# Kernel tuning notes

Measured on AMD Instinct MI355X. Metric: run time of the kernel, lower is better.

Reference implementation:

```python
import jax, jax.numpy as jnp
import numpy as np

N_NODES = 50000
N_EDGES = 600000
N_GRAPHS = 64


def _linear_init(key, fan_in, fan_out):
    # torch nn.Linear default: U(-1/sqrt(fan_in), 1/sqrt(fan_in))
    s = 1.0 / np.sqrt(fan_in)
    kw, kb = jax.random.split(key)
    W = jax.random.uniform(kw, (fan_in, fan_out), jnp.float32, -s, s)
    b = jax.random.uniform(kb, (fan_out,), jnp.float32, -s, s)
    return W, b


def setup_inputs() -> dict:
    key = jax.random.key(0)
    ks = jax.random.split(key, 7)
    x = jax.random.normal(ks[0], (N_NODES, 128), jnp.float32)
    edge_index = jax.random.randint(ks[1], (2, N_EDGES), 0, N_NODES, dtype=jnp.int32).astype(jnp.int64)
    batch = jnp.sort(jax.random.randint(ks[2], (N_NODES,), 0, N_GRAPHS, dtype=jnp.int32)).astype(jnp.int64)
    W1, b1 = _linear_init(ks[3], 128, 256)
    W2, b2 = _linear_init(ks[4], 256, 256)
    W3, b3 = _linear_init(ks[5], 256, 128)
    W4, b4 = _linear_init(ks[6], 128, 10)
    return dict(x=x, edge_index=edge_index, batch=batch,
                W1=W1, b1=b1, W2=W2, b2=b2, W3=W3, b3=b3, W4=W4, b4=b4)


def _gcn_conv(h, src, dst, W, b, n_nodes):
    # PyG GCNConv: add self-loops (src/dst already include them),
    # symmetric normalization D^{-1/2} (A+I) D^{-1/2} h W + b.
    h = h @ W                                      # [N, Cout]
    deg = jax.ops.segment_sum(jnp.ones(src.shape[0], h.dtype), dst, num_segments=n_nodes)
    dinv = jnp.where(deg > 0, jax.lax.rsqrt(deg), 0.0)
    norm = dinv[src] * dinv[dst]                   # [E+N]
    msg = h[src] * norm[:, None]                   # gather + scale per edge
    agg = jax.ops.segment_sum(msg, dst, num_segments=n_nodes)  # scatter-add
    return agg + b


def reference(x, edge_index, batch, W1, b1, W2, b2, W3, b3, W4, b4):
    n = x.shape[0]
    loops = jnp.arange(n, dtype=edge_index.dtype)
    src = jnp.concatenate([edge_index[0], loops])
    dst = jnp.concatenate([edge_index[1], loops])
    # GCNBlock (activate_last=True since dense layers follow)
    h = jax.nn.relu(_gcn_conv(x, src, dst, W1, b1, n))
    h = jax.nn.relu(_gcn_conv(h, src, dst, W2, b2, n))
    # global_mean_pool over batch segments
    sums = jax.ops.segment_sum(h, batch, num_segments=N_GRAPHS)          # [G, 256]
    counts = jax.ops.segment_sum(jnp.ones((n,), h.dtype), batch, num_segments=N_GRAPHS)
    g = sums / jnp.maximum(counts, 1.0)[:, None]
    # DenseBlock [256 -> 128 -> 10], activate_last=False
    g = jax.nn.relu(g @ W3 + b3)
    return g @ W4 + b4
```

## Files before the change

### kernel.cpp

```cpp
#include <hip/hip_runtime.h>

typedef unsigned short u16;
typedef unsigned int u32;
typedef __attribute__((ext_vector_type(8))) short s16x8;
typedef __attribute__((ext_vector_type(4))) float f32x4;

#define NN 50000
#define NE 600000
#define NG 64

__device__ __forceinline__ u16 f2bf(float f) {
    u32 u = __float_as_uint(f);
    u32 r = (u + 0x7fffu + ((u >> 16) & 1u)) >> 16;
    return (u16)r;
}
__device__ __forceinline__ float bf2f(u16 h) {
    return __uint_as_float(((u32)h) << 16);
}
__device__ __forceinline__ void gll16(const void* g, void* l) {
    __builtin_amdgcn_global_load_lds((const __attribute__((address_space(1))) u32*)g,
                                     (__attribute__((address_space(3))) u32*)l, 16, 0, 0);
}

__global__ void k_hist(const int* __restrict__ dst, int* __restrict__ cnt, int ne) {
    int e = blockIdx.x * blockDim.x + threadIdx.x;
    if (e < ne) atomicAdd(&cnt[dst[e]], 1);
}

__global__ __launch_bounds__(256)
void k_scan1(const int* __restrict__ cnt, int* __restrict__ bsum, int n) {
    int i = blockIdx.x * 256 + threadIdx.x;
    int v = (i < n) ? cnt[i] : 0;
#pragma unroll
    for (int off = 32; off > 0; off >>= 1) v += __shfl_down(v, off, 64);
    __shared__ int ws[4];
    int lane = threadIdx.x & 63, w = threadIdx.x >> 6;
    if (lane == 0) ws[w] = v;
    __syncthreads();
    if (threadIdx.x == 0) bsum[blockIdx.x] = ws[0] + ws[1] + ws[2] + ws[3];
}

__global__ __launch_bounds__(256)
void k_scan2(int* __restrict__ bsum, int nb) {
    int t = threadIdx.x;
    int v = (t < nb) ? bsum[t] : 0;
    int lane = t & 63, w = t >> 6;
    int inc = v;
#pragma unroll
    for (int off = 1; off < 64; off <<= 1) {
        int x = __shfl_up(inc, off, 64);
        if (lane >= off) inc += x;
    }
    __shared__ int wtot[4];
    if (lane == 63) wtot[w] = inc;
    __syncthreads();
    int wo = 0;
    for (int j = 0; j < w; ++j) wo += wtot[j];
    if (t < nb) bsum[t] = wo + inc - v;
}

__global__ __launch_bounds__(256)
void k_scan3(const int* __restrict__ cnt, const int* __restrict__ boff,
             int* __restrict__ rowptr, int* __restrict__ cursor,
             float* __restrict__ dinv, int n) {
    int i = blockIdx.x * 256 + threadIdx.x;
    int v = (i < n) ? cnt[i] : 0;
    int lane = threadIdx.x & 63, w = threadIdx.x >> 6;
    int inc = v;
#pragma unroll
    for (int off = 1; off < 64; off <<= 1) {
        int x = __shfl_up(inc, off, 64);
        if (lane >= off) inc += x;
    }
    __shared__ int wtot[4];
    if (lane == 63) wtot[w] = inc;
    __syncthreads();
    int wo = boff[blockIdx.x];
    for (int j = 0; j < w; ++j) wo += wtot[j];
    if (i < n) {
        int excl = wo + inc - v;
        rowptr[i] = excl;
        cursor[i] = excl;
        dinv[i] = rsqrtf(1.0f + (float)v);
        if (i == n - 1) rowptr[n] = excl + v;
    }
}

__global__ void k_fill(const int* __restrict__ src, const int* __restrict__ dst,
                       const float* __restrict__ dinv,
                       int* __restrict__ cursor, uint2* __restrict__ csr2, int ne) {
    int e = blockIdx.x * blockDim.x + threadIdx.x;
    if (e < ne) {
        int pos = atomicAdd(&cursor[dst[e]], 1);
        int s = src[e];
        csr2[pos] = make_uint2((u32)s, __float_as_uint(dinv[s]));
    }
}

__device__ __forceinline__ void wsplit_tiled(const float* __restrict__ W,
                                             u16* __restrict__ hi, int gid) {
    int n = gid & 255, kgrp = gid >> 8;
    int kbase = kgrp * 8;
#pragma unroll
    for (int j = 0; j < 8; ++j) {
        float w = W[(size_t)(kbase + j) * 256 + n];
        hi[(size_t)gid * 8 + j] = f2bf(w);
    }
}

__global__ __launch_bounds__(256)
void k_preamble(const float* __restrict__ x, u16* __restrict__ xbf,
                const float* __restrict__ W1, u16* __restrict__ w1hi,
                const float* __restrict__ W2, u16* __restrict__ w2hi,
                float* __restrict__ sums, int* __restrict__ cnt,
                const int* __restrict__ batch, float* __restrict__ counts) {
    const int XB = (NN * 32 + 255) / 256;
    const int CB = (NN + 255) / 256;
    int b = blockIdx.x, t = threadIdx.x;
    if (b < XB) {
        int i = b * 256 + t;
        if (i < NN * 32) {
            float4 v = ((const float4*)x)[i];
            ushort4 o;
            o.x = f2bf(v.x); o.y = f2bf(v.y); o.z = f2bf(v.z); o.w = f2bf(v.w);
            ((ushort4*)xbf)[i] = o;
        }
        return;
    }
    b -= XB;
    if (b < 16) { wsplit_tiled(W1, w1hi, b * 256 + t); return; }
    b -= 16;
    if (b < 32) { wsplit_tiled(W2, w2hi, b * 256 + t); return; }
    b -= 32;
    if (b < 64) { sums[b * 256 + t] = 0.f; return; }
    b -= 64;
    if (b < CB) {
        int i = b * 256 + t;
        if (i < NN) cnt[i] = 0;
        return;
    }
    b -= CB;
    if (b == 0) {
        __shared__ int lb[65];
        if (t <= 64) {
            int lo = 0, hi = NN;
            while (lo < hi) {
                int mid = (lo + hi) >> 1;
                if (batch[mid] < t) lo = mid + 1; else hi = mid;
            }
            lb[t] = lo;
        }
        __syncthreads();
        if (t < 64) counts[t] = (float)(lb[t + 1] - lb[t]);
    }
}

__device__ __forceinline__ void fma8(float* a, const uint4& v, float w) {
    a[0] += bf2f((u16)v.x) * w; a[1] += bf2f((u16)(v.x >> 16)) * w;
    a[2] += bf2f((u16)v.y) * w; a[3] += bf2f((u16)(v.y >> 16)) * w;
    a[4] += bf2f((u16)v.z) * w; a[5] += bf2f((u16)(v.z >> 16)) * w;
    a[6] += bf2f((u16)v.w) * w; a[7] += bf2f((u16)(v.w >> 16)) * w;
}
__device__ __forceinline__ void fma4(float* a, const uint2& v, float w) {
    a[0] += bf2f((u16)v.x) * w; a[1] += bf2f((u16)(v.x >> 16)) * w;
    a[2] += bf2f((u16)v.y) * w; a[3] += bf2f((u16)(v.y >> 16)) * w;
}

template<int C>
__global__ __launch_bounds__(256)
void k_agg_gather(const int* __restrict__ rowptr, const uint2* __restrict__ csr2,
                  const float* __restrict__ dinv, const u16* __restrict__ hb,
                  u16* __restrict__ out, int n) {
    constexpr int VL = C / 32;
    int tid = threadIdx.x;
    int node = (blockIdx.x * 256 + tid) >> 5;
    if (node >= n) return;
    int sl = tid & 31;
    int beg = rowptr[node];
    int m = rowptr[node + 1] - beg;
    float di = dinv[node];
    float a0[VL], a1[VL];
    if constexpr (VL == 8) {
        uint4 v = ((const uint4*)hb)[(size_t)node * 32 + sl];
#pragma unroll
        for (int i = 0; i < 8; ++i) a1[i] = 0.f;
        a0[0] = bf2f((u16)v.x) * di; a0[1] = bf2f((u16)(v.x >> 16)) * di;
        a0[2] = bf2f((u16)v.y) * di; a0[3] = bf2f((u16)(v.y >> 16)) * di;
        a0[4] = bf2f((u16)v.z) * di; a0[5] = bf2f((u16)(v.z >> 16)) * di;
        a0[6] = bf2f((u16)v.w) * di; a0[7] = bf2f((u16)(v.w >> 16)) * di;
    } else {
        uint2 v = ((const uint2*)hb)[(size_t)node * 32 + sl];
#pragma unroll
        for (int i = 0; i < 4; ++i) a1[i] = 0.f;
        a0[0] = bf2f((u16)v.x) * di; a0[1] = bf2f((u16)(v.x >> 16)) * di;
        a0[2] = bf2f((u16)v.y) * di; a0[3] = bf2f((u16)(v.y >> 16)) * di;
    }
    const uint2* ep = csr2 + beg;
    int e = 0;
    for (; e + 4 <= m; e += 4) {
        uint2 e0 = ep[e], e1 = ep[e + 1], e2 = ep[e + 2], e3 = ep[e + 3];
        float w0 = __uint_as_float(e0.y), w1 = __uint_as_float(e1.y);
        float w2 = __uint_as_float(e2.y), w3 = __uint_as_float(e3.y);
        if constexpr (VL == 8) {
            uint4 r0 = ((const uint4*)hb)[(size_t)e0.x * 32 + sl];
            uint4 r1 = ((const uint4*)hb)[(size_t)e1.x * 32 + sl];
            uint4 r2 = ((const uint4*)hb)[(size_t)e2.x * 32 + sl];
            uint4 r3 = ((const uint4*)hb)[(size_t)e3.x * 32 + sl];
            fma8(a0, r0, w0); fma8(a1, r1, w1); fma8(a0, r2, w2); fma8(a1, r3, w3);
        } else {
            uint2 r0 = ((const uint2*)hb)[(size_t)e0.x * 32 + sl];
            uint2 r1 = ((const uint2*)hb)[(size_t)e1.x * 32 + sl];
            uint2 r2 = ((const uint2*)hb)[(size_t)e2.x * 32 + sl];
            uint2 r3 = ((const uint2*)hb)[(size_t)e3.x * 32 + sl];
            fma4(a0, r0, w0); fma4(a1, r1, w1); fma4(a0, r2, w2); fma4(a1, r3, w3);
        }
    }
    for (; e < m; ++e) {
        uint2 e0 = ep[e];
        float w0 = __uint_as_float(e0.y);
        if constexpr (VL == 8) {
            uint4 r0 = ((const uint4*)hb)[(size_t)e0.x * 32 + sl];
            fma8(a0, r0, w0);
        } else {
            uint2 r0 = ((const uint2*)hb)[(size_t)e0.x * 32 + sl];
            fma4(a0, r0, w0);
        }
    }
    if constexpr (VL == 8) {
        uint4 o;
        o.x = (u32)f2bf((a0[0] + a1[0]) * di) | ((u32)f2bf((a0[1] + a1[1]) * di) << 16);
        o.y = (u32)f2bf((a0[2] + a1[2]) * di) | ((u32)f2bf((a0[3] + a1[3]) * di) << 16);
        o.z = (u32)f2bf((a0[4] + a1[4]) * di) | ((u32)f2bf((a0[5] + a1[5]) * di) << 16);
        o.w = (u32)f2bf((a0[6] + a1[6]) * di) | ((u32)f2bf((a0[7] + a1[7]) * di) << 16);
        ((uint4*)out)[(size_t)node * 32 + sl] = o;
    } else {
        uint2 o;
        o.x = (u32)f2bf((a0[0] + a1[0]) * di) | ((u32)f2bf((a0[1] + a1[1]) * di) << 16);
        o.y = (u32)f2bf((a0[2] + a1[2]) * di) | ((u32)f2bf((a0[3] + a1[3]) * di) << 16);
        ((uint2*)out)[(size_t)node * 32 + sl] = o;
    }
}

template<bool POOL>
__global__ __launch_bounds__(512, 4)
void k_gemm_mfma(const u16* __restrict__ A, const u16* __restrict__ Bh,
                 const float* __restrict__ bias, u16* __restrict__ out_bf,
                 const int* __restrict__ batch, float* __restrict__ pool,
                 int M, int K) {
    __shared__ u16 ldsA[2][4096];
    const int tid = threadIdx.x, lane = tid & 63, wid = tid >> 6;
    const int bm = blockIdx.x * 128;
    const int wr = (wid >> 2) * 64, wc = (wid & 3) * 64;
    const int lr = lane & 15, kg = lane >> 4;

    const int srow = wid * 16 + (lane >> 2);
    const int sslot = lane & 3;
    const int ssw = (srow ^ (srow >> 2)) & 3;
    int srg = bm + srow; if (srg >= M) srg = M - 1;
    const u16* sbase = A + (size_t)srg * K + ((sslot ^ ssw) << 3);

    const u16* bh_p = Bh + (u32)kg * 2048 + (u32)(wc + lr) * 8;

    f32x4 acc[4][4];
#pragma unroll
    for (int i = 0; i < 4; ++i)
#pragma unroll
        for (int j = 0; j < 4; ++j) acc[i][j] = (f32x4){0.f, 0.f, 0.f, 0.f};

    const int nt = K >> 5;
    gll16(sbase, &ldsA[0][wid * 512]);
    __syncthreads();

    for (int t = 0; t < nt; ++t) {
        int cur = t & 1;
        if (t + 1 < nt)
            gll16(sbase + ((t + 1) << 5), &ldsA[cur ^ 1][wid * 512]);

        s16x8 bh[4];
#pragma unroll
        for (int fn = 0; fn < 4; ++fn)
            bh[fn] = *(const s16x8*)&bh_p[(u32)t * 8192 + (u32)fn * 128];
        const u16* lb = ldsA[cur];
        s16x8 a[4];
#pragma unroll
        for (int fm = 0; fm < 4; ++fm) {
            int r = wr + fm * 16 + lr;
            a[fm] = *(const s16x8*)&lb[r * 32 + ((kg ^ ((r ^ (r >> 2)) & 3)) << 3)];
        }
#pragma unroll
        for (int fn = 0; fn < 4; ++fn)
#pragma unroll
            for (int fm = 0; fm < 4; ++fm)
                acc[fm][fn] = __builtin_amdgcn_mfma_f32_16x16x32_bf16(a[fm], bh[fn], acc[fm][fn], 0, 0, 0);
        __syncthreads();
    }

#pragma unroll
    for (int fn = 0; fn < 4; ++fn) {
        int col = wc + fn * 16 + lr;
        float bv = bias[col];
        if (!POOL) {
#pragma unroll
            for (int fm = 0; fm < 4; ++fm) {
                int rbase = bm + wr + fm * 16 + kg * 4;
#pragma unroll
                for (int r = 0; r < 4; ++r) {
                    int row = rbase + r;
                    if (row < M)
                        out_bf[(size_t)row * 256 + col] = f2bf(fmaxf(acc[fm][fn][r] + bv, 0.f));
                }
            }
        } else {
            int gcur = -1;
            float run = 0.f;
#pragma unroll
            for (int fm = 0; fm < 4; ++fm) {
                int rbase = bm + wr + fm * 16 + kg * 4;
#pragma unroll
                for (int r = 0; r < 4; ++r) {
                    int row = rbase + r;
                    if (row < M) {
                        int g = batch[row];
                        float v = fmaxf(acc[fm][fn][r] + bv, 0.f);
                        if (g != gcur) {
                            if (gcur >= 0) atomicAdd(&pool[gcur * 256 + col], run);
                            gcur = g;
                            run = 0.f;
                        }
                        run += v;
                    }
                }
            }
            if (gcur >= 0) atomicAdd(&pool[gcur * 256 + col], run);
        }
    }
}

__global__ __launch_bounds__(128)
void k_dense(const float* __restrict__ sums, const float* __restrict__ counts,
             const float* __restrict__ W3, const float* __restrict__ b3,
             const float* __restrict__ W4, const float* __restrict__ b4,
             float* __restrict__ out) {
    __shared__ float g[256];
    __shared__ float hid[128];
    int gi = blockIdx.x;
    int t = threadIdx.x;
    float inv = 1.0f / fmaxf(counts[gi], 1.0f);
    for (int c = t; c < 256; c += 128) g[c] = sums[gi * 256 + c] * inv;
    __syncthreads();
    float acc = b3[t];
    for (int k = 0; k < 256; ++k) acc += g[k] * W3[k * 128 + t];
    hid[t] = fmaxf(acc, 0.0f);
    __syncthreads();
    if (t < 10) {
        float o = b4[t];
        for (int k = 0; k < 128; ++k) o += hid[k] * W4[k * 10 + t];
        out[gi * 10 + t] = o;
    }
}

extern "C" void kernel_launch(void* const* d_in, const int* in_sizes, int n_in,
                              void* d_out, int out_size, void* d_ws, size_t ws_size,
                              hipStream_t stream) {
    const float* x   = (const float*)d_in[0];
    const int*  eidx = (const int*)d_in[1];
    const int*  batch= (const int*)d_in[2];
    const float* W1 = (const float*)d_in[3];
    const float* b1 = (const float*)d_in[4];
    const float* W2 = (const float*)d_in[5];
    const float* b2 = (const float*)d_in[6];
    const float* W3 = (const float*)d_in[7];
    const float* b3 = (const float*)d_in[8];
    const float* W4 = (const float*)d_in[9];
    const float* b4 = (const float*)d_in[10];
    float* out = (float*)d_out;

    const int N = NN, E = NE, G = NG;
    const int* src = eidx;
    const int* dst = eidx + E;
    const int NB = (N + 255) / 256;

    char* p = (char*)d_ws;
    auto alloc = [&](size_t bytes) { char* r = p; p += (bytes + 255) & ~(size_t)255; return r; };
    u16*   h1bf   = (u16*)alloc((size_t)N * 256 * 2);
    u16*   xbf    = (u16*)alloc((size_t)N * 128 * 2);
    float* dinv   = (float*)alloc((size_t)N * 4);
    float* sums   = (float*)alloc((size_t)G * 256 * 4);
    float* counts = (float*)alloc((size_t)G * 4);
    int*   cnt    = (int*)alloc((size_t)N * 4);
    int*   rowptr = (int*)alloc((size_t)(N + 1) * 4);
    int*   bsum   = (int*)alloc((size_t)NB * 4);
    uint2* csr2   = (uint2*)alloc((size_t)E * 8);
    u16*   agg1   = (u16*)alloc((size_t)N * 128 * 2);
    u16*   agg2   = (u16*)alloc((size_t)N * 256 * 2);
    u16*   w1hi   = (u16*)alloc((size_t)256 * 128 * 2);
    u16*   w2hi   = (u16*)alloc((size_t)256 * 256 * 2);
    int*   cursor = cnt;

    const int XB = (NN * 32 + 255) / 256;
    const int CB = (NN + 255) / 256;
    int pre_blocks = XB + 16 + 32 + 64 + CB + 1;
    k_preamble<<<pre_blocks, 256, 0, stream>>>(x, xbf, W1, w1hi, W2, w2hi,
                                               sums, cnt, batch, counts);

    k_hist<<<(E + 255) / 256, 256, 0, stream>>>(dst, cnt, E);
    k_scan1<<<NB, 256, 0, stream>>>(cnt, bsum, N);
    k_scan2<<<1, 256, 0, stream>>>(bsum, NB);
    k_scan3<<<NB, 256, 0, stream>>>(cnt, bsum, rowptr, cursor, dinv, N);
    k_fill<<<(E + 255) / 256, 256, 0, stream>>>(src, dst, dinv, cursor, csr2, E);

    k_agg_gather<128><<<(N + 7) / 8, 256, 0, stream>>>(rowptr, csr2, dinv, xbf, agg1, N);
    int gblocks = (N + 127) / 128;
    k_gemm_mfma<false><<<gblocks, 512, 0, stream>>>(agg1, w1hi, b1, h1bf,
                                                    nullptr, nullptr, N, 128);

    k_agg_gather<256><<<(N + 7) / 8, 256, 0, stream>>>(rowptr, csr2, dinv, h1bf, agg2, N);
    k_gemm_mfma<true><<<gblocks, 512, 0, stream>>>(agg2, w2hi, b2, nullptr,
                                                   batch, sums, N, 256);

    k_dense<<<G, 128, 0, stream>>>(sums, counts, W3, b3, W4, b4, out);
}
```

Measured before the change: 215.3 us.

## Fuse neighbor aggregation into MFMA GEMM via LDS-resident aggregated tile

Merges the sparse gather-aggregate kernel with the following MFMA GEMM: each 512-thread block aggregates its 128 nodes directly into a swizzled LDS tile holding the full K width, then runs the GEMM from LDS without double-buffered global loads. This removes the write and re-read of the intermediate aggregated feature buffers and two kernel launches. In exchange, LDS use grows to 64 KB for K=256, which may cut occupancy, and the irregular gather phase no longer overlaps with MFMA work inside a block.

New measurement: 220.5 us. 1.02x slower.

```diff
diff --git a/kernel.cpp b/kernel.cpp
--- a/kernel.cpp
+++ b/kernel.cpp
@@ -16,10 +16,6 @@
 }
 __device__ __forceinline__ float bf2f(u16 h) {
     return __uint_as_float(((u32)h) << 16);
-}
-__device__ __forceinline__ void gll16(const void* g, void* l) {
-    __builtin_amdgcn_global_load_lds((const __attribute__((address_space(1))) u32*)g,
-                                     (__attribute__((address_space(3))) u32*)l, 16, 0, 0);
 }
 
 __global__ void k_hist(const int* __restrict__ dst, int* __restrict__ cnt, int ne) {
@@ -166,99 +162,95 @@
     a[2] += bf2f((u16)v.y) * w; a[3] += bf2f((u16)(v.y >> 16)) * w;
 }
 
-template<int C>
-__global__ __launch_bounds__(256)
-void k_agg_gather(const int* __restrict__ rowptr, const uint2* __restrict__ csr2,
-                  const float* __restrict__ dinv, const u16* __restrict__ hb,
-                  u16* __restrict__ out, int n) {
-    constexpr int VL = C / 32;
-    int tid = threadIdx.x;
-    int node = (blockIdx.x * 256 + tid) >> 5;
-    if (node >= n) return;
-    int sl = tid & 31;
-    int beg = rowptr[node];
-    int m = rowptr[node + 1] - beg;
-    float di = dinv[node];
-    float a0[VL], a1[VL];
-    if constexpr (VL == 8) {
-        uint4 v = ((const uint4*)hb)[(size_t)node * 32 + sl];
-#pragma unroll
-        for (int i = 0; i < 8; ++i) a1[i] = 0.f;
-        a0[0] = bf2f((u16)v.x) * di; a0[1] = bf2f((u16)(v.x >> 16)) * di;
-        a0[2] = bf2f((u16)v.y) * di; a0[3] = bf2f((u16)(v.y >> 16)) * di;
-        a0[4] = bf2f((u16)v.z) * di; a0[5] = bf2f((u16)(v.z >> 16)) * di;
-        a0[6] = bf2f((u16)v.w) * di; a0[7] = bf2f((u16)(v.w >> 16)) * di;
-    } else {
-        uint2 v = ((const uint2*)hb)[(size_t)node * 32 + sl];
-#pragma unroll
-        for (int i = 0; i < 4; ++i) a1[i] = 0.f;
-        a0[0] = bf2f((u16)v.x) * di; a0[1] = bf2f((u16)(v.x >> 16)) * di;
-        a0[2] = bf2f((u16)v.y) * di; a0[3] = bf2f((u16)(v.y >> 16)) * di;
-    }
-    const uint2* ep = csr2 + beg;
-    int e = 0;
-    for (; e + 4 <= m; e += 4) {
-        uint2 e0 = ep[e], e1 = ep[e + 1], e2 = ep[e + 2], e3 = ep[e + 3];
-        float w0 = __uint_as_float(e0.y), w1 = __uint_as_float(e1.y);
-        float w2 = __uint_as_float(e2.y), w3 = __uint_as_float(e3.y);
-        if constexpr (VL == 8) {
-            uint4 r0 = ((const uint4*)hb)[(size_t)e0.x * 32 + sl];
-            uint4 r1 = ((const uint4*)hb)[(size_t)e1.x * 32 + sl];
-            uint4 r2 = ((const uint4*)hb)[(size_t)e2.x * 32 + sl];
-            uint4 r3 = ((const uint4*)hb)[(size_t)e3.x * 32 + sl];
-            fma8(a0, r0, w0); fma8(a1, r1, w1); fma8(a0, r2, w2); fma8(a1, r3, w3);
-        } else {
-            uint2 r0 = ((const uint2*)hb)[(size_t)e0.x * 32 + sl];
-            uint2 r1 = ((const uint2*)hb)[(size_t)e1.x * 32 + sl];
-            uint2 r2 = ((const uint2*)hb)[(size_t)e2.x * 32 + sl];
-            uint2 r3 = ((const uint2*)hb)[(size_t)e3.x * 32 + sl];
-            fma4(a0, r0, w0); fma4(a1, r1, w1); fma4(a0, r2, w2); fma4(a1, r3, w3);
-        }
-    }
-    for (; e < m; ++e) {
-        uint2 e0 = ep[e];
-        float w0 = __uint_as_float(e0.y);
-        if constexpr (VL == 8) {
-            uint4 r0 = ((const uint4*)hb)[(size_t)e0.x * 32 + sl];
-            fma8(a0, r0, w0);
-        } else {
-            uint2 r0 = ((const uint2*)hb)[(size_t)e0.x * 32 + sl];
-            fma4(a0, r0, w0);
-        }
-    }
-    if constexpr (VL == 8) {
-        uint4 o;
-        o.x = (u32)f2bf((a0[0] + a1[0]) * di) | ((u32)f2bf((a0[1] + a1[1]) * di) << 16);
-        o.y = (u32)f2bf((a0[2] + a1[2]) * di) | ((u32)f2bf((a0[3] + a1[3]) * di) << 16);
-        o.z = (u32)f2bf((a0[4] + a1[4]) * di) | ((u32)f2bf((a0[5] + a1[5]) * di) << 16);
-        o.w = (u32)f2bf((a0[6] + a1[6]) * di) | ((u32)f2bf((a0[7] + a1[7]) * di) << 16);
-        ((uint4*)out)[(size_t)node * 32 + sl] = o;
-    } else {
-        uint2 o;
-        o.x = (u32)f2bf((a0[0] + a1[0]) * di) | ((u32)f2bf((a0[1] + a1[1]) * di) << 16);
-        o.y = (u32)f2bf((a0[2] + a1[2]) * di) | ((u32)f2bf((a0[3] + a1[3]) * di) << 16);
-        ((uint2*)out)[(size_t)node * 32 + sl] = o;
-    }
-}
-
-template<bool POOL>
+template<bool POOL, int K>
 __global__ __launch_bounds__(512, 4)
-void k_gemm_mfma(const u16* __restrict__ A, const u16* __restrict__ Bh,
-                 const float* __restrict__ bias, u16* __restrict__ out_bf,
-                 const int* __restrict__ batch, float* __restrict__ pool,
-                 int M, int K) {
-    __shared__ u16 ldsA[2][4096];
+void k_fused(const int* __restrict__ rowptr, const uint2* __restrict__ csr2,
+             const float* __restrict__ dinv, const u16* __restrict__ hb,
+             const u16* __restrict__ Bh, const float* __restrict__ bias,
+             u16* __restrict__ out_bf, const int* __restrict__ batch,
+             float* __restrict__ pool, int M) {
+    __shared__ u16 ldsA[128 * K];
     const int tid = threadIdx.x, lane = tid & 63, wid = tid >> 6;
     const int bm = blockIdx.x * 128;
+    constexpr int VL = K / 32;
+
+    {
+        int sl = lane & 31;
+        int half = lane >> 5;
+        for (int it = 0; it < 8; ++it) {
+            int row = wid * 16 + it * 2 + half;
+            int node = bm + row; if (node >= M) node = M - 1;
+            int beg = rowptr[node];
+            int m = rowptr[node + 1] - beg;
+            float di = dinv[node];
+            float a0[VL], a1[VL];
+            if constexpr (VL == 8) {
+                uint4 v = ((const uint4*)hb)[(size_t)node * 32 + sl];
+#pragma unroll
+                for (int i = 0; i < 8; ++i) a1[i] = 0.f;
+                a0[0] = bf2f((u16)v.x) * di; a0[1] = bf2f((u16)(v.x >> 16)) * di;
+                a0[2] = bf2f((u16)v.y) * di; a0[3] = bf2f((u16)(v.y >> 16)) * di;
+                a0[4] = bf2f((u16)v.z) * di; a0[5] = bf2f((u16)(v.z >> 16)) * di;
+                a0[6] = bf2f((u16)v.w) * di; a0[7] = bf2f((u16)(v.w >> 16)) * di;
+            } else {
+                uint2 v = ((const uint2*)hb)[(size_t)node * 32 + sl];
+#pragma unroll
+                for (int i = 0; i < 4; ++i) a1[i] = 0.f;
+                a0[0] = bf2f((u16)v.x) * di; a0[1] = bf2f((u16)(v.x >> 16)) * di;
+                a0[2] = bf2f((u16)v.y) * di; a0[3] = bf2f((u16)(v.y >> 16)) * di;
+            }
+            const uint2* ep = csr2 + beg;
+            int e = 0;
+            for (; e + 4 <= m; e += 4) {
+                uint2 e0 = ep[e], e1 = ep[e + 1], e2 = ep[e + 2], e3 = ep[e + 3];
+                float w0 = __uint_as_float(e0.y), w1 = __uint_as_float(e1.y);
+                float w2 = __uint_as_float(e2.y), w3 = __uint_as_float(e3.y);
+                if constexpr (VL == 8) {
+                    uint4 r0 = ((const uint4*)hb)[(size_t)e0.x * 32 + sl];
+                    uint4 r1 = ((const uint4*)hb)[(size_t)e1.x * 32 + sl];
+                    uint4 r2 = ((const uint4*)hb)[(size_t)e2.x * 32 + sl];
+                    uint4 r3 = ((const uint4*)hb)[(size_t)e3.x * 32 + sl];
+                    fma8(a0, r0, w0); fma8(a1, r1, w1); fma8(a0, r2, w2); fma8(a1, r3, w3);
+                } else {
+                    uint2 r0 = ((const uint2*)hb)[(size_t)e0.x * 32 + sl];
+                    uint2 r1 = ((const uint2*)hb)[(size_t)e1.x * 32 + sl];
+                    uint2 r2 = ((const uint2*)hb)[(size_t)e2.x * 32 + sl];
+                    uint2 r3 = ((const uint2*)hb)[(size_t)e3.x * 32 + sl];
+                    fma4(a0, r0, w0); fma4(a1, r1, w1); fma4(a0, r2, w2); fma4(a1, r3, w3);
+                }
+            }
+            for (; e < m; ++e) {
+                uint2 e0 = ep[e];
+                float w0 = __uint_as_float(e0.y);
+                if constexpr (VL == 8) {
+                    uint4 r0 = ((const uint4*)hb)[(size_t)e0.x * 32 + sl];
+                    fma8(a0, r0, w0);
+                } else {
+                    uint2 r0 = ((const uint2*)hb)[(size_t)e0.x * 32 + sl];
+                    fma4(a0, r0, w0);
+                }
+            }
+            int swzr = (row ^ (row >> 2)) & 3;
+            if constexpr (VL == 8) {
+                uint4 o;
+                o.x = (u32)f2bf((a0[0] + a1[0]) * di) | ((u32)f2bf((a0[1] + a1[1]) * di) << 16);
+                o.y = (u32)f2bf((a0[2] + a1[2]) * di) | ((u32)f2bf((a0[3] + a1[3]) * di) << 16);
+                o.z = (u32)f2bf((a0[4] + a1[4]) * di) | ((u32)f2bf((a0[5] + a1[5]) * di) << 16);
+                o.w = (u32)f2bf((a0[6] + a1[6]) * di) | ((u32)f2bf((a0[7] + a1[7]) * di) << 16);
+                *(uint4*)&ldsA[row * K + ((sl ^ swzr) << 3)] = o;
+            } else {
+                uint2 o;
+                o.x = (u32)f2bf((a0[0] + a1[0]) * di) | ((u32)f2bf((a0[1] + a1[1]) * di) << 16);
+                o.y = (u32)f2bf((a0[2] + a1[2]) * di) | ((u32)f2bf((a0[3] + a1[3]) * di) << 16);
+                int slot = sl >> 1, hf = sl & 1;
+                *(uint2*)&ldsA[row * K + (((slot ^ swzr) << 3) + hf * 4)] = o;
+            }
+        }
+    }
+    __syncthreads();
+
     const int wr = (wid >> 2) * 64, wc = (wid & 3) * 64;
     const int lr = lane & 15, kg = lane >> 4;
-
-    const int srow = wid * 16 + (lane >> 2);
-    const int sslot = lane & 3;
-    const int ssw = (srow ^ (srow >> 2)) & 3;
-    int srg = bm + srow; if (srg >= M) srg = M - 1;
-    const u16* sbase = A + (size_t)srg * K + ((sslot ^ ssw) << 3);
-
     const u16* bh_p = Bh + (u32)kg * 2048 + (u32)(wc + lr) * 8;
 
     f32x4 acc[4][4];
@@ -267,32 +259,24 @@
 #pragma unroll
         for (int j = 0; j < 4; ++j) acc[i][j] = (f32x4){0.f, 0.f, 0.f, 0.f};
 
-    const int nt = K >> 5;
-    gll16(sbase, &ldsA[0][wid * 512]);
-    __syncthreads();
-
+    constexpr int nt = K >> 5;
+#pragma unroll
     for (int t = 0; t < nt; ++t) {
-        int cur = t & 1;
-        if (t + 1 < nt)
-            gll16(sbase + ((t + 1) << 5), &ldsA[cur ^ 1][wid * 512]);
-
         s16x8 bh[4];
 #pragma unroll
         for (int fn = 0; fn < 4; ++fn)
             bh[fn] = *(const s16x8*)&bh_p[(u32)t * 8192 + (u32)fn * 128];
-        const u16* lb = ldsA[cur];
         s16x8 a[4];
 #pragma unroll
         for (int fm = 0; fm < 4; ++fm) {
             int r = wr + fm * 16 + lr;
-            a[fm] = *(const s16x8*)&lb[r * 32 + ((kg ^ ((r ^ (r >> 2)) & 3)) << 3)];
+            a[fm] = *(const s16x8*)&ldsA[r * K + (((t * 4 + kg) ^ ((r ^ (r >> 2)) & 3)) << 3)];
         }
 #pragma unroll
         for (int fn = 0; fn < 4; ++fn)
 #pragma unroll
             for (int fm = 0; fm < 4; ++fm)
                 acc[fm][fn] = __builtin_amdgcn_mfma_f32_16x16x32_bf16(a[fm], bh[fn], acc[fm][fn], 0, 0, 0);
-        __syncthreads();
     }
 
 #pragma unroll
@@ -391,8 +375,6 @@
     int*   rowptr = (int*)alloc((size_t)(N + 1) * 4);
     int*   bsum   = (int*)alloc((size_t)NB * 4);
     uint2* csr2   = (uint2*)alloc((size_t)E * 8);
-    u16*   agg1   = (u16*)alloc((size_t)N * 128 * 2);
-    u16*   agg2   = (u16*)alloc((size_t)N * 256 * 2);
     u16*   w1hi   = (u16*)alloc((size_t)256 * 128 * 2);
     u16*   w2hi   = (u16*)alloc((size_t)256 * 256 * 2);
     int*   cursor = cnt;
@@ -409,14 +391,11 @@
     k_scan3<<<NB, 256, 0, stream>>>(cnt, bsum, rowptr, cursor, dinv, N);
     k_fill<<<(E + 255) / 256, 256, 0, stream>>>(src, dst, dinv, cursor, csr2, E);
 
-    k_agg_gather<128><<<(N + 7) / 8, 256, 0, stream>>>(rowptr, csr2, dinv, xbf, agg1, N);
     int gblocks = (N + 127) / 128;
-    k_gemm_mfma<false><<<gblocks, 512, 0, stream>>>(agg1, w1hi, b1, h1bf,
-                                                    nullptr, nullptr, N, 128);
-
-    k_agg_gather<256><<<(N + 7) / 8, 256, 0, stream>>>(rowptr, csr2, dinv, h1bf, agg2, N);
-    k_gemm_mfma<true><<<gblocks, 512, 0, stream>>>(agg2, w2hi, b2, nullptr,
-                                                   batch, sums, N, 256);
+    k_fused<false, 128><<<gblocks, 512, 0, stream>>>(rowptr, csr2, dinv, xbf, w1hi, b1,
+                                                     h1bf, nullptr, nullptr, N);
+    k_fused<true, 256><<<gblocks, 512, 0, stream>>>(rowptr, csr2, dinv, h1bf, w2hi, b2,
+                                                    nullptr, batch, sums, N);
 
     k_dense<<<G, 128, 0, stream>>>(sums, counts, W3, b3, W4, b4, out);
 }
```
